# Optimization experiments

Measured on AMD Instinct MI355X. Metric: run time of the kernel, lower is better.

Reference implementation:

```python
import jax, jax.numpy as jnp
import numpy as np

N_LVL = 127.0   # 8-bit symmetric: 2**(8-1) - 1
BN_EPS = 1e-5
PATCH = 16


def quant_act(x):
    """Per-tensor 8-bit symmetric quant-dequant (HAWQ-style QuantAct, dynamic range)."""
    scale = jnp.max(jnp.abs(x)) / N_LVL
    xq = jnp.clip(jnp.round(x / scale), -N_LVL, N_LVL) * scale
    return xq, scale


def setup_inputs() -> dict:
    key = jax.random.key(0)
    k0, k1, k2, k3, k4 = jax.random.split(key, 5)
    B, C, H = 128, 3, 224
    dim = 768
    x = jax.random.normal(k0, (B, C, H, H), jnp.float32)
    W = jax.random.normal(k1, (dim, C, PATCH, PATCH), jnp.float32) * 0.02
    b = jax.random.normal(k2, (dim,), jnp.float32) * 0.02
    gamma = jnp.ones((dim,), jnp.float32)
    beta = jnp.zeros((dim,), jnp.float32)
    run_mean = jax.random.normal(k3, (dim,), jnp.float32) * 0.1
    run_var = jax.random.uniform(k4, (dim,), jnp.float32, 0.5, 1.5)
    return {"x": x, "W": W, "b": b, "gamma": gamma, "beta": beta,
            "run_mean": run_mean, "run_var": run_var}


def reference(x, W, b, gamma, beta, run_mean, run_var):
    # --- quant_input ---
    x_q, pre_s = quant_act(x)                                   # [B,3,224,224], scalar
    # --- QuantConv2d: per-out-channel 8-bit symmetric weight quant ---
    w_scale = jnp.max(jnp.abs(W), axis=(1, 2, 3), keepdims=True) / N_LVL  # [dim,1,1,1]
    w_int = jnp.round(W / w_scale)
    x_int = x_q / pre_s                                         # integer-valued activations
    comb_s = w_scale[:, 0, 0, 0] * pre_s                        # [dim] conv output scale
    b_int = jnp.round(b / comb_s)
    y = jax.lax.conv_general_dilated(
        x_int, w_int, window_strides=(PATCH, PATCH), padding='VALID',
        dimension_numbers=('NCHW', 'OIHW', 'NCHW'))             # [B,768,14,14]
    y = (y + b_int[None, :, None, None]) * comb_s[None, :, None, None]
    # --- quant_act_conv ---
    y, _ = quant_act(y)
    # --- GELU (torch nn.GELU default: exact erf) ---
    y = jax.nn.gelu(y, approximate=False)
    # --- qact1 ---
    y, _ = quant_act(y)
    # --- BatchNorm2d (eval mode, running stats) ---
    inv = gamma / jnp.sqrt(run_var + BN_EPS)
    y = y * inv[None, :, None, None] + (beta - run_mean * inv)[None, :, None, None]
    # --- qact2 ---
    y, act_scale = quant_act(y)
    return y, act_scale
```

## Files before the change

kernel.cpp:

```cpp
#include <hip/hip_runtime.h>

#define TOT   19267584
#define MROWS 25088
#define KD    768
#define NPB   196
#define CHW   150528

typedef unsigned int uint;
typedef __attribute__((ext_vector_type(4))) int i32x4;

#define OFF_AQ   0ull
#define OFF_WQ   19267584ull
#define OFF_WSC  19857408ull
#define OFF_INV  19860480ull
#define OFF_SHF  19863552ull
#define OFF_PA   19866624ull
#define OFF_PB   19871328ull
#define OFF_CMN  19880736ull
#define OFF_CMX  19886880ull

__device__ __forceinline__ float wave_max(float v) {
#pragma unroll
  for (int off = 32; off > 0; off >>= 1) v = fmaxf(v, __shfl_xor(v, off));
  return v;
}

__device__ __forceinline__ float block_max(float v) {
  __shared__ float red[4];
  v = wave_max(v);
  __syncthreads();
  if ((threadIdx.x & 63) == 0) red[threadIdx.x >> 6] = v;
  __syncthreads();
  return fmaxf(fmaxf(red[0], red[1]), fmaxf(red[2], red[3]));
}

__global__ void k_max_wq(const float* __restrict__ x, float* __restrict__ pA,
                         const float* __restrict__ W, const float* __restrict__ gamma,
                         const float* __restrict__ beta, const float* __restrict__ rmean,
                         const float* __restrict__ rvar, signed char* __restrict__ wq,
                         float* __restrict__ wscale, float* __restrict__ inv_,
                         float* __restrict__ shf) {
  if (blockIdx.x < 1176) {
    const int i0 = blockIdx.x * 256 + threadIdx.x;
    const float4* x4 = (const float4*)x;
    float m = 0.f;
#pragma unroll
    for (int j = 0; j < 16; j += 4) {
      float4 a = x4[i0 + (j + 0) * 301056];
      float4 b = x4[i0 + (j + 1) * 301056];
      float4 c = x4[i0 + (j + 2) * 301056];
      float4 d = x4[i0 + (j + 3) * 301056];
      m = fmaxf(m, fmaxf(fmaxf(fabsf(a.x), fabsf(a.y)), fmaxf(fabsf(a.z), fabsf(a.w))));
      m = fmaxf(m, fmaxf(fmaxf(fabsf(b.x), fabsf(b.y)), fmaxf(fabsf(b.z), fabsf(b.w))));
      m = fmaxf(m, fmaxf(fmaxf(fabsf(c.x), fabsf(c.y)), fmaxf(fabsf(c.z), fabsf(c.w))));
      m = fmaxf(m, fmaxf(fmaxf(fabsf(d.x), fabsf(d.y)), fmaxf(fabsf(d.z), fabsf(d.w))));
    }
    float bm = block_max(m);
    if (threadIdx.x == 0) pA[blockIdx.x] = bm;
  } else {
    const int oc = blockIdx.x - 1176;
    const float* row = W + oc * KD;
    float m = 0.f;
    for (int k = threadIdx.x; k < KD; k += 256) m = fmaxf(m, fabsf(row[k]));
    const float ws_ = block_max(m) / 127.0f;
    for (int k = threadIdx.x; k < KD; k += 256)
      wq[oc * KD + k] = (signed char)(int)rintf(row[k] / ws_);
    if (threadIdx.x == 0) {
      wscale[oc] = ws_;
      float iv = gamma[oc] / sqrtf(rvar[oc] + 1e-5f);
      inv_[oc] = iv;
      shf[oc] = __fsub_rn(beta[oc], __fmul_rn(rmean[oc], iv));
    }
  }
}

__global__ void k_im2col(const float* __restrict__ x, const float* __restrict__ pA,
                         signed char* __restrict__ aq) {
  float mm = 0.f;
  for (int i = threadIdx.x; i < 1176; i += 256) mm = fmaxf(mm, pA[i]);
  const float ps = block_max(mm) / 127.0f;
  const int u = blockIdx.x * 256 + threadIdx.x;
  const int p = u / 48, r = u - p * 48;
  const int c = r >> 4, kh = r & 15;
  const int b = p / NPB, pp = p - b * NPB;
  const int ph = pp / 14, pw = pp - ph * 14;
  const float* src = x + (((b * 3 + c) * 224 + ph * 16 + kh) * 224 + pw * 16);
  float4 v0 = *(const float4*)(src);
  float4 v1 = *(const float4*)(src + 4);
  float4 v2 = *(const float4*)(src + 8);
  float4 v3 = *(const float4*)(src + 12);
#define Q8(v) ((int)fminf(fmaxf(rintf((v) / ps), -127.f), 127.f) & 255)
  uint4 o;
  o.x = Q8(v0.x) | (Q8(v0.y) << 8) | (Q8(v0.z) << 16) | ((uint)Q8(v0.w) << 24);
  o.y = Q8(v1.x) | (Q8(v1.y) << 8) | (Q8(v1.z) << 16) | ((uint)Q8(v1.w) << 24);
  o.z = Q8(v2.x) | (Q8(v2.y) << 8) | (Q8(v2.z) << 16) | ((uint)Q8(v2.w) << 24);
  o.w = Q8(v3.x) | (Q8(v3.y) << 8) | (Q8(v3.z) << 16) | ((uint)Q8(v3.w) << 24);
#undef Q8
  *(uint4*)(aq + (size_t)p * KD + (r << 4)) = o;
}

__device__ __forceinline__ void gl_lds16(const void* g, void* l) {
  __builtin_amdgcn_global_load_lds((const __attribute__((address_space(1))) void*)g,
                                   (__attribute__((address_space(3))) void*)l, 16, 0, 0);
}

__global__ __launch_bounds__(256) void k_gemm(const signed char* __restrict__ aq,
                                              const signed char* __restrict__ wq,
                                              const float* __restrict__ bias,
                                              const float* __restrict__ wscale,
                                              const float* __restrict__ pA,
                                              float* __restrict__ y,
                                              float* __restrict__ pB) {
  __shared__ __align__(16) signed char L[3][12288];
  const int tid = threadIdx.x, lane = tid & 63, wv = tid >> 6;
  const int bsw = (blockIdx.x & 7) * 294 + (blockIdx.x >> 3);
  const int bm = bsw / 6, bn = bsw - 6 * (bsw / 6);
  const int wr = wv >> 1, wc = wv & 1;

  const int bo = (((lane & 3) ^ ((lane >> 3) & 3)) << 4);
#define SRC(c) ((c) < 4 ? aq + (size_t)(bm * 64 + (c) * 16 + (lane >> 2)) * KD + bo \
                        : wq + (size_t)(bn * 128 + ((c) - 4) * 16 + (lane >> 2)) * KD + bo)
  const int c0 = wv * 3, c1 = wv * 3 + 1, c2 = wv * 3 + 2;
  const signed char* g0 = SRC(c0);
  const signed char* g1 = SRC(c1);
  const signed char* g2 = SRC(c2);
#undef SRC

  i32x4 acc[2][4];
#pragma unroll
  for (int m = 0; m < 2; ++m)
#pragma unroll
    for (int n = 0; n < 4; ++n) acc[m][n] = (i32x4){0, 0, 0, 0};

  const int rbase = lane & 15;
  const int kg = ((lane >> 4) << 4) ^ (((lane >> 1) & 3) << 4);

#define STAGE(T, B)                                   \
  {                                                   \
    const int kk_ = (T) * 64;                         \
    gl_lds16(g0 + kk_, &L[B][c0 * 1024]);             \
    gl_lds16(g1 + kk_, &L[B][c1 * 1024]);             \
    gl_lds16(g2 + kk_, &L[B][c2 * 1024]);             \
  }

  STAGE(0, 0)
  STAGE(1, 1)
#pragma unroll
  for (int t = 0; t < 12; ++t) {
    if (t < 11) { asm volatile("s_waitcnt vmcnt(3)" ::: "memory"); }
    else        { asm volatile("s_waitcnt vmcnt(0)" ::: "memory"); }
    __builtin_amdgcn_s_barrier();
    __builtin_amdgcn_sched_barrier(0);
    const int b = t % 3;
    i32x4 af[2], bfr[4];
#pragma unroll
    for (int m = 0; m < 2; ++m)
      af[m] = *(const i32x4*)&L[b][(wr * 32 + m * 16 + rbase) * 64 + kg];
#pragma unroll
    for (int n = 0; n < 4; ++n)
      bfr[n] = *(const i32x4*)&L[b][4096 + (wc * 64 + n * 16 + rbase) * 64 + kg];
    if (t < 10) STAGE(t + 2, (t + 2) % 3)
#pragma unroll
    for (int m = 0; m < 2; ++m)
#pragma unroll
      for (int n = 0; n < 4; ++n)
        acc[m][n] = __builtin_amdgcn_mfma_i32_16x16x64_i8(af[m], bfr[n], acc[m][n], 0, 0, 0);
  }
#undef STAGE

  float mm = 0.f;
  for (int i = tid; i < 1176; i += 256) mm = fmaxf(mm, pA[i]);
  const float ps = block_max(mm) / 127.0f;

  float lmax = 0.f;
  const int prow = (lane >> 4) << 2;
#pragma unroll
  for (int n = 0; n < 4; ++n) {
    const int oc = bn * 128 + wc * 64 + n * 16 + rbase;
    const float comb = wscale[oc] * ps;
    const float bint = rintf(bias[oc] / comb);
#pragma unroll
    for (int m = 0; m < 2; ++m) {
      const int p0 = bm * 64 + wr * 32 + m * 16 + prow;
      const int img = p0 / 196;
      const int q = p0 - img * 196;
      float4 o;
      o.x = ((float)acc[m][n][0] + bint) * comb;
      o.y = ((float)acc[m][n][1] + bint) * comb;
      o.z = ((float)acc[m][n][2] + bint) * comb;
      o.w = ((float)acc[m][n][3] + bint) * comb;
      lmax = fmaxf(lmax, fmaxf(fmaxf(fabsf(o.x), fabsf(o.y)), fmaxf(fabsf(o.z), fabsf(o.w))));
      *(float4*)(y + (size_t)img * CHW + (size_t)oc * 196 + q) = o;
    }
  }
  float bm_ = block_max(lmax);
  if (tid == 0) pB[blockIdx.x] = bm_;
}

__global__ void k_gelu_chan(const float* __restrict__ y, const float* __restrict__ pB,
                            signed char* __restrict__ k1, float* __restrict__ cmn2,
                            float* __restrict__ cmx2) {
  const int c = blockIdx.x >> 1, half = blockIdx.x & 1;
  float mm = 0.f;
  for (int i = threadIdx.x; i < 2352; i += 256) mm = fmaxf(mm, pB[i]);
  const float s1 = block_max(mm) / 127.0f;
  __shared__ float tab[255];
  for (int t = threadIdx.x; t < 255; t += 256) {
    float y1 = (float)(t - 127) * s1;
    float e = erff(y1 * 0.70710678118654752f);
    tab[t] = (y1 * (e + 1.0f)) * 0.5f;
  }
  __syncthreads();
  float mn = 1e30f, mx = -1e30f;
  const float4* y4 = (const float4*)y;
  char4* k4 = (char4*)k1;
#define ADDR(u) ((size_t)(half * 64 + (u) / 49) * (CHW / 4) + (size_t)c * 49 + ((u) - ((u) / 49) * 49))
#define PROC(v, a4)                                                        \
  {                                                                        \
    int ia = (int)fminf(fmaxf(rintf((v).x / s1), -127.f), 127.f);          \
    int ib = (int)fminf(fmaxf(rintf((v).y / s1), -127.f), 127.f);          \
    int ic = (int)fminf(fmaxf(rintf((v).z / s1), -127.f), 127.f);          \
    int id = (int)fminf(fmaxf(rintf((v).w / s1), -127.f), 127.f);          \
    char4 kk;                                                              \
    kk.x = (signed char)ia; kk.y = (signed char)ib;                        \
    kk.z = (signed char)ic; kk.w = (signed char)id;                        \
    k4[a4] = kk;                                                           \
    float ga = tab[ia + 127], gb = tab[ib + 127];                          \
    float gc = tab[ic + 127], gd = tab[id + 127];                          \
    mn = fminf(mn, fminf(fminf(ga, gb), fminf(gc, gd)));                   \
    mx = fmaxf(mx, fmaxf(fmaxf(ga, gb), fmaxf(gc, gd)));                   \
  }
  for (int r = 0; r < 3; ++r) {
    const int u0 = threadIdx.x + r * 1024;
    const size_t a0 = ADDR(u0), a1 = ADDR(u0 + 256), a2 = ADDR(u0 + 512), a3 = ADDR(u0 + 768);
    float4 v0 = y4[a0];
    float4 v1 = y4[a1];
    float4 v2 = y4[a2];
    float4 v3 = y4[a3];
    PROC(v0, a0) PROC(v1, a1) PROC(v2, a2) PROC(v3, a3)
  }
  if (threadIdx.x < 64) {
    const int u = 3072 + threadIdx.x;
    const size_t a = ADDR(u);
    float4 v = y4[a];
    PROC(v, a)
  }
#undef PROC
#undef ADDR
  __shared__ float rmn[4], rmx[4];
#pragma unroll
  for (int off = 32; off > 0; off >>= 1) {
    mn = fminf(mn, __shfl_xor(mn, off));
    mx = fmaxf(mx, __shfl_xor(mx, off));
  }
  const int lane = threadIdx.x & 63, wvx = threadIdx.x >> 6;
  if (lane == 0) { rmn[wvx] = mn; rmx[wvx] = mx; }
  __syncthreads();
  if (threadIdx.x == 0) {
    cmn2[blockIdx.x] = fminf(fminf(rmn[0], rmn[1]), fminf(rmn[2], rmn[3]));
    cmx2[blockIdx.x] = fmaxf(fmaxf(rmx[0], rmx[1]), fmaxf(rmx[2], rmx[3]));
  }
}

__global__ void k_final(const signed char* __restrict__ k1, const float* __restrict__ pB,
                        const float* __restrict__ cmn2, const float* __restrict__ cmx2,
                        const float* __restrict__ inv_, const float* __restrict__ shf,
                        float* __restrict__ out) {
  float mm = 0.f;
  for (int i = threadIdx.x; i < 2352; i += 256) mm = fmaxf(mm, pB[i]);
  const float s1 = block_max(mm) / 127.0f;
  float m2 = 0.f;
  for (int i = threadIdx.x; i < 1536; i += 256)
    m2 = fmaxf(m2, fmaxf(fabsf(cmn2[i]), fabsf(cmx2[i])));
  const float s2 = block_max(m2) / 127.0f;
  float m4 = 0.f;
  for (int c = threadIdx.x; c < 768; c += 256) {
    float mn = fminf(cmn2[2 * c], cmn2[2 * c + 1]);
    float mx = fmaxf(cmx2[2 * c], cmx2[2 * c + 1]);
    float iv = inv_[c], sh = shf[c];
    float a = fminf(fmaxf(rintf(mn / s2), -127.f), 127.f) * s2;
    float b = fminf(fmaxf(rintf(mx / s2), -127.f), 127.f) * s2;
    float ya = __fadd_rn(__fmul_rn(a, iv), sh);
    float yb = __fadd_rn(__fmul_rn(b, iv), sh);
    m4 = fmaxf(m4, fmaxf(fabsf(ya), fabsf(yb)));
  }
  const float s3 = block_max(m4) / 127.0f;

  __shared__ float tab[255];
  for (int t = threadIdx.x; t < 255; t += 256) {
    float y1 = (float)(t - 127) * s1;
    float e = erff(y1 * 0.70710678118654752f);
    float y2 = (y1 * (e + 1.0f)) * 0.5f;
    float q2 = fminf(fmaxf(rintf(y2 / s2), -127.f), 127.f);
    tab[t] = q2 * s2;
  }
  __syncthreads();
  const int i = blockIdx.x * 256 + threadIdx.x;
  const char4* k4 = (const char4*)k1;
  char4 a0 = k4[i];
  char4 a1 = k4[i + 1204224];
  char4 a2 = k4[i + 2 * 1204224];
  char4 a3 = k4[i + 3 * 1204224];
  float4* out4 = (float4*)out;
#define FIN(kk, idx)                                                       \
  {                                                                        \
    int c = ((idx) / 49) % 768;                                            \
    float iv = inv_[c], sh = shf[c];                                       \
    float fa = __fadd_rn(__fmul_rn(tab[kk.x + 127], iv), sh);              \
    float fb = __fadd_rn(__fmul_rn(tab[kk.y + 127], iv), sh);              \
    float fc = __fadd_rn(__fmul_rn(tab[kk.z + 127], iv), sh);              \
    float fd = __fadd_rn(__fmul_rn(tab[kk.w + 127], iv), sh);              \
    float4 o;                                                              \
    o.x = fminf(fmaxf(rintf(fa / s3), -127.f), 127.f) * s3;                \
    o.y = fminf(fmaxf(rintf(fb / s3), -127.f), 127.f) * s3;                \
    o.z = fminf(fmaxf(rintf(fc / s3), -127.f), 127.f) * s3;                \
    o.w = fminf(fmaxf(rintf(fd / s3), -127.f), 127.f) * s3;                \
    out4[idx] = o;                                                         \
  }
  FIN(a0, i)
  FIN(a1, i + 1204224)
  FIN(a2, i + 2 * 1204224)
  FIN(a3, i + 3 * 1204224)
#undef FIN
  if (blockIdx.x == 0 && threadIdx.x == 0) out[TOT] = s3;
}

extern "C" void kernel_launch(void* const* d_in, const int* in_sizes, int n_in,
                              void* d_out, int out_size, void* d_ws, size_t ws_size,
                              hipStream_t stream) {
  const float* x     = (const float*)d_in[0];
  const float* W     = (const float*)d_in[1];
  const float* bias  = (const float*)d_in[2];
  const float* gamma = (const float*)d_in[3];
  const float* beta  = (const float*)d_in[4];
  const float* rmean = (const float*)d_in[5];
  const float* rvar  = (const float*)d_in[6];
  float* out = (float*)d_out;
  char* ws = (char*)d_ws;

  signed char* aq  = (signed char*)(ws + OFF_AQ);
  signed char* wq  = (signed char*)(ws + OFF_WQ);
  float* wsc  = (float*)(ws + OFF_WSC);
  float* inv_ = (float*)(ws + OFF_INV);
  float* shf  = (float*)(ws + OFF_SHF);
  float* pA   = (float*)(ws + OFF_PA);
  float* pB   = (float*)(ws + OFF_PB);
  float* cmn2 = (float*)(ws + OFF_CMN);
  float* cmx2 = (float*)(ws + OFF_CMX);
  signed char* k1 = (signed char*)(ws + OFF_AQ);

  k_max_wq<<<1944, 256, 0, stream>>>(x, pA, W, gamma, beta, rmean, rvar, wq, wsc, inv_, shf);
  k_im2col<<<4704, 256, 0, stream>>>(x, pA, aq);
  k_gemm<<<2352, 256, 0, stream>>>(aq, wq, bias, wsc, pA, out, pB);
  k_gelu_chan<<<1536, 256, 0, stream>>>(out, pB, k1, cmn2, cmx2);
  k_final<<<4704, 256, 0, stream>>>(k1, pB, cmn2, cmx2, inv_, shf, out);
}
```

Before: 128.0 us.

## Fuse im2col quantization into GEMM with register-resident A tile

Drops the separate im2col kernel. Each GEMM block now quantizes its own 32 patch rows straight from x into LDS and holds the whole K=768 A fragment in registers. The block then loops over all six 128-column N tiles, streaming weights through a double-buffered LDS stage. This removes the int8 activation write/read round trip and one launch. In exchange the grid is smaller (784 blocks), a full barrier runs every k-step, and register use is higher.

```diff
diff --git a/kernel.cpp b/kernel.cpp
--- a/kernel.cpp
+++ b/kernel.cpp
@@ -9,7 +9,7 @@
 typedef unsigned int uint;
 typedef __attribute__((ext_vector_type(4))) int i32x4;
 
-#define OFF_AQ   0ull
+#define OFF_K1   0ull
 #define OFF_WQ   19267584ull
 #define OFF_WSC  19857408ull
 #define OFF_INV  19860480ull
@@ -74,125 +74,121 @@
   }
 }
 
-__global__ void k_im2col(const float* __restrict__ x, const float* __restrict__ pA,
-                         signed char* __restrict__ aq) {
-  float mm = 0.f;
-  for (int i = threadIdx.x; i < 1176; i += 256) mm = fmaxf(mm, pA[i]);
-  const float ps = block_max(mm) / 127.0f;
-  const int u = blockIdx.x * 256 + threadIdx.x;
-  const int p = u / 48, r = u - p * 48;
-  const int c = r >> 4, kh = r & 15;
-  const int b = p / NPB, pp = p - b * NPB;
-  const int ph = pp / 14, pw = pp - ph * 14;
-  const float* src = x + (((b * 3 + c) * 224 + ph * 16 + kh) * 224 + pw * 16);
-  float4 v0 = *(const float4*)(src);
-  float4 v1 = *(const float4*)(src + 4);
-  float4 v2 = *(const float4*)(src + 8);
-  float4 v3 = *(const float4*)(src + 12);
-#define Q8(v) ((int)fminf(fmaxf(rintf((v) / ps), -127.f), 127.f) & 255)
-  uint4 o;
-  o.x = Q8(v0.x) | (Q8(v0.y) << 8) | (Q8(v0.z) << 16) | ((uint)Q8(v0.w) << 24);
-  o.y = Q8(v1.x) | (Q8(v1.y) << 8) | (Q8(v1.z) << 16) | ((uint)Q8(v1.w) << 24);
-  o.z = Q8(v2.x) | (Q8(v2.y) << 8) | (Q8(v2.z) << 16) | ((uint)Q8(v2.w) << 24);
-  o.w = Q8(v3.x) | (Q8(v3.y) << 8) | (Q8(v3.z) << 16) | ((uint)Q8(v3.w) << 24);
-#undef Q8
-  *(uint4*)(aq + (size_t)p * KD + (r << 4)) = o;
-}
-
 __device__ __forceinline__ void gl_lds16(const void* g, void* l) {
   __builtin_amdgcn_global_load_lds((const __attribute__((address_space(1))) void*)g,
                                    (__attribute__((address_space(3))) void*)l, 16, 0, 0);
 }
 
-__global__ __launch_bounds__(256) void k_gemm(const signed char* __restrict__ aq,
+__global__ __launch_bounds__(256) void k_gemm(const float* __restrict__ x,
                                               const signed char* __restrict__ wq,
                                               const float* __restrict__ bias,
                                               const float* __restrict__ wscale,
                                               const float* __restrict__ pA,
                                               float* __restrict__ y,
                                               float* __restrict__ pB) {
-  __shared__ __align__(16) signed char L[3][12288];
+  __shared__ signed char aL[32 * 784];
+  __shared__ __align__(16) signed char bL[2][8192];
   const int tid = threadIdx.x, lane = tid & 63, wv = tid >> 6;
-  const int bsw = (blockIdx.x & 7) * 294 + (blockIdx.x >> 3);
-  const int bm = bsw / 6, bn = bsw - 6 * (bsw / 6);
+  const int bm = blockIdx.x;
   const int wr = wv >> 1, wc = wv & 1;
-
-  const int bo = (((lane & 3) ^ ((lane >> 3) & 3)) << 4);
-#define SRC(c) ((c) < 4 ? aq + (size_t)(bm * 64 + (c) * 16 + (lane >> 2)) * KD + bo \
-                        : wq + (size_t)(bn * 128 + ((c) - 4) * 16 + (lane >> 2)) * KD + bo)
-  const int c0 = wv * 3, c1 = wv * 3 + 1, c2 = wv * 3 + 2;
-  const signed char* g0 = SRC(c0);
-  const signed char* g1 = SRC(c1);
-  const signed char* g2 = SRC(c2);
-#undef SRC
-
-  i32x4 acc[2][4];
-#pragma unroll
-  for (int m = 0; m < 2; ++m)
-#pragma unroll
-    for (int n = 0; n < 4; ++n) acc[m][n] = (i32x4){0, 0, 0, 0};
-
-  const int rbase = lane & 15;
-  const int kg = ((lane >> 4) << 4) ^ (((lane >> 1) & 3) << 4);
-
-#define STAGE(T, B)                                   \
-  {                                                   \
-    const int kk_ = (T) * 64;                         \
-    gl_lds16(g0 + kk_, &L[B][c0 * 1024]);             \
-    gl_lds16(g1 + kk_, &L[B][c1 * 1024]);             \
-    gl_lds16(g2 + kk_, &L[B][c2 * 1024]);             \
-  }
-
-  STAGE(0, 0)
-  STAGE(1, 1)
-#pragma unroll
-  for (int t = 0; t < 12; ++t) {
-    if (t < 11) { asm volatile("s_waitcnt vmcnt(3)" ::: "memory"); }
-    else        { asm volatile("s_waitcnt vmcnt(0)" ::: "memory"); }
-    __builtin_amdgcn_s_barrier();
-    __builtin_amdgcn_sched_barrier(0);
-    const int b = t % 3;
-    i32x4 af[2], bfr[4];
-#pragma unroll
-    for (int m = 0; m < 2; ++m)
-      af[m] = *(const i32x4*)&L[b][(wr * 32 + m * 16 + rbase) * 64 + kg];
-#pragma unroll
-    for (int n = 0; n < 4; ++n)
-      bfr[n] = *(const i32x4*)&L[b][4096 + (wc * 64 + n * 16 + rbase) * 64 + kg];
-    if (t < 10) STAGE(t + 2, (t + 2) % 3)
-#pragma unroll
-    for (int m = 0; m < 2; ++m)
-#pragma unroll
-      for (int n = 0; n < 4; ++n)
-        acc[m][n] = __builtin_amdgcn_mfma_i32_16x16x64_i8(af[m], bfr[n], acc[m][n], 0, 0, 0);
-  }
-#undef STAGE
 
   float mm = 0.f;
   for (int i = tid; i < 1176; i += 256) mm = fmaxf(mm, pA[i]);
   const float ps = block_max(mm) / 127.0f;
 
+  {
+    const int tq = tid & 127;
+    const int pl = tq >> 2, pc = tq & 3;
+    const int p = bm * 32 + pl;
+    const int img = p / 196, pp = p - img * 196;
+    const int ph = pp / 14, pw = pp - ph * 14;
+    const float* xb = x + ((size_t)img * 3 * 224 + ph * 16) * 224 + pw * 16;
+#pragma unroll
+    for (int it = 0; it < 6; ++it) {
+      const int ks = it * 2 + (tid >> 7);
+      const int k = ks * 64 + pc * 16;
+      const int cch = k >> 8, kh = (k >> 4) & 15;
+      const float* src = xb + ((size_t)cch * 224 + kh) * 224;
+      float4 v0 = *(const float4*)(src);
+      float4 v1 = *(const float4*)(src + 4);
+      float4 v2 = *(const float4*)(src + 8);
+      float4 v3 = *(const float4*)(src + 12);
+#define Q8(v) ((int)fminf(fmaxf(rintf((v) / ps), -127.f), 127.f) & 255)
+      uint4 o;
+      o.x = Q8(v0.x) | (Q8(v0.y) << 8) | (Q8(v0.z) << 16) | ((uint)Q8(v0.w) << 24);
+      o.y = Q8(v1.x) | (Q8(v1.y) << 8) | (Q8(v1.z) << 16) | ((uint)Q8(v1.w) << 24);
+      o.z = Q8(v2.x) | (Q8(v2.y) << 8) | (Q8(v2.z) << 16) | ((uint)Q8(v2.w) << 24);
+      o.w = Q8(v3.x) | (Q8(v3.y) << 8) | (Q8(v3.z) << 16) | ((uint)Q8(v3.w) << 24);
+#undef Q8
+      *(uint4*)&aL[pl * 784 + ks * 64 + pc * 16] = o;
+    }
+  }
+
+  const int ci0 = wv * 2, ci1 = wv * 2 + 1;
+  const int bo = (((lane & 3) ^ ((lane >> 3) & 3)) << 4);
+  const signed char* gB0 = wq + (size_t)(ci0 * 16 + (lane >> 2)) * KD + bo;
+  const signed char* gB1 = wq + (size_t)(ci1 * 16 + (lane >> 2)) * KD + bo;
+#define STAGE(BN, KS, B)                                        \
+  {                                                             \
+    const int off_ = (BN) * 98304 + (KS) * 64;                  \
+    gl_lds16(gB0 + off_, &bL[B][ci0 * 1024]);                   \
+    gl_lds16(gB1 + off_, &bL[B][ci1 * 1024]);                   \
+  }
+
+  STAGE(0, 0, 0)
+  __syncthreads();
+
+  const int rbase = lane & 15;
+  const int kg16 = (lane >> 4) << 4;
+  i32x4 af[12];
+#pragma unroll
+  for (int ks = 0; ks < 12; ++ks)
+    af[ks] = *(const i32x4*)&aL[(wr * 16 + rbase) * 784 + ks * 64 + kg16];
+
+  const int kg = kg16 ^ (((lane >> 1) & 3) << 4);
+  const int prow = (lane >> 4) << 2;
+  const int p0 = bm * 32 + wr * 16 + prow;
+  const int img = p0 / 196;
+  const int q = p0 - img * 196;
+  float* ybase = y + (size_t)img * CHW + q;
+
   float lmax = 0.f;
-  const int prow = (lane >> 4) << 2;
-#pragma unroll
-  for (int n = 0; n < 4; ++n) {
-    const int oc = bn * 128 + wc * 64 + n * 16 + rbase;
-    const float comb = wscale[oc] * ps;
-    const float bint = rintf(bias[oc] / comb);
-#pragma unroll
-    for (int m = 0; m < 2; ++m) {
-      const int p0 = bm * 64 + wr * 32 + m * 16 + prow;
-      const int img = p0 / 196;
-      const int q = p0 - img * 196;
+  i32x4 acc[4];
+#pragma unroll
+  for (int n = 0; n < 4; ++n) acc[n] = (i32x4){0, 0, 0, 0};
+
+  for (int bn = 0; bn < 6; ++bn) {
+#pragma unroll
+    for (int ks = 0; ks < 12; ++ks) {
+      const int buf = ks & 1;
+      i32x4 bfr[4];
+#pragma unroll
+      for (int n = 0; n < 4; ++n)
+        bfr[n] = *(const i32x4*)&bL[buf][(wc * 64 + n * 16 + rbase) * 64 + kg];
+      if (ks < 11) STAGE(bn, ks + 1, buf ^ 1)
+      else if (bn < 5) STAGE(bn + 1, 0, buf ^ 1)
+#pragma unroll
+      for (int n = 0; n < 4; ++n)
+        acc[n] = __builtin_amdgcn_mfma_i32_16x16x64_i8(af[ks], bfr[n], acc[n], 0, 0, 0);
+      __syncthreads();
+    }
+#pragma unroll
+    for (int n = 0; n < 4; ++n) {
+      const int oc = bn * 128 + wc * 64 + n * 16 + rbase;
+      const float comb = wscale[oc] * ps;
+      const float bint = rintf(bias[oc] / comb);
       float4 o;
-      o.x = ((float)acc[m][n][0] + bint) * comb;
-      o.y = ((float)acc[m][n][1] + bint) * comb;
-      o.z = ((float)acc[m][n][2] + bint) * comb;
-      o.w = ((float)acc[m][n][3] + bint) * comb;
+      o.x = ((float)acc[n][0] + bint) * comb;
+      o.y = ((float)acc[n][1] + bint) * comb;
+      o.z = ((float)acc[n][2] + bint) * comb;
+      o.w = ((float)acc[n][3] + bint) * comb;
       lmax = fmaxf(lmax, fmaxf(fmaxf(fabsf(o.x), fabsf(o.y)), fmaxf(fabsf(o.z), fabsf(o.w))));
-      *(float4*)(y + (size_t)img * CHW + (size_t)oc * 196 + q) = o;
-    }
-  }
+      *(float4*)(ybase + (size_t)oc * 196) = o;
+      acc[n] = (i32x4){0, 0, 0, 0};
+    }
+  }
+#undef STAGE
+
   float bm_ = block_max(lmax);
   if (tid == 0) pB[blockIdx.x] = bm_;
 }
@@ -202,7 +198,7 @@
                             float* __restrict__ cmx2) {
   const int c = blockIdx.x >> 1, half = blockIdx.x & 1;
   float mm = 0.f;
-  for (int i = threadIdx.x; i < 2352; i += 256) mm = fmaxf(mm, pB[i]);
+  for (int i = threadIdx.x; i < 784; i += 256) mm = fmaxf(mm, pB[i]);
   const float s1 = block_max(mm) / 127.0f;
   __shared__ float tab[255];
   for (int t = threadIdx.x; t < 255; t += 256) {
@@ -267,7 +263,7 @@
                         const float* __restrict__ inv_, const float* __restrict__ shf,
                         float* __restrict__ out) {
   float mm = 0.f;
-  for (int i = threadIdx.x; i < 2352; i += 256) mm = fmaxf(mm, pB[i]);
+  for (int i = threadIdx.x; i < 784; i += 256) mm = fmaxf(mm, pB[i]);
   const float s1 = block_max(mm) / 127.0f;
   float m2 = 0.f;
   for (int i = threadIdx.x; i < 1536; i += 256)
@@ -338,7 +334,6 @@
   float* out = (float*)d_out;
   char* ws = (char*)d_ws;
 
-  signed char* aq  = (signed char*)(ws + OFF_AQ);
   signed char* wq  = (signed char*)(ws + OFF_WQ);
   float* wsc  = (float*)(ws + OFF_WSC);
   float* inv_ = (float*)(ws + OFF_INV);
@@ -347,11 +342,10 @@
   float* pB   = (float*)(ws + OFF_PB);
   float* cmn2 = (float*)(ws + OFF_CMN);
   float* cmx2 = (float*)(ws + OFF_CMX);
-  signed char* k1 = (signed char*)(ws + OFF_AQ);
+  signed char* k1 = (signed char*)(ws + OFF_K1);
 
   k_max_wq<<<1944, 256, 0, stream>>>(x, pA, W, gamma, beta, rmean, rvar, wq, wsc, inv_, shf);
-  k_im2col<<<4704, 256, 0, stream>>>(x, pA, aq);
-  k_gemm<<<2352, 256, 0, stream>>>(aq, wq, bias, wsc, pA, out, pB);
+  k_gemm<<<784, 256, 0, stream>>>(x, wq, bias, wsc, pA, out, pB);
   k_gelu_chan<<<1536, 256, 0, stream>>>(out, pB, k1, cmn2, cmx2);
   k_final<<<4704, 256, 0, stream>>>(k1, pB, cmn2, cmx2, inv_, shf, out);
 }
```

New measurement: 150.7 us. 17.7% more time.
